# Kernel tuning notes

Hardware: AMD Instinct MI355X
Metric: run time of the kernel (lower is better)

The kernel has to match this reference:

```python
import jax, jax.numpy as jnp
import numpy as np

EPS = 1e-5  # BatchNorm2d default eps


def setup_inputs() -> dict:
    key = jax.random.key(0)
    k1, k2, k3, k4 = jax.random.split(key, 4)
    B, C, S, E = 2, 512, 256, 512  # C == E is required by the module's math
    x = jax.random.normal(k1, (B, C, S, E), dtype=jnp.float32)
    Q = jax.random.normal(k2, (E, E), dtype=jnp.float32)
    K = jax.random.normal(k3, (E, E), dtype=jnp.float32)
    V = jax.random.normal(k4, (E, E), dtype=jnp.float32)
    return {"x": x, "Q": Q, "K": K, "V": V}


def reference(x, Q, K, V):
    # BatchNorm2d(affine=False), training-mode batch stats over (B, H, W)
    mean = jnp.mean(x, axis=(0, 2, 3), keepdims=True)
    var = jnp.var(x, axis=(0, 2, 3), keepdims=True)  # biased, matches torch normalization
    xn = (x - mean) * jax.lax.rsqrt(var + EPS)

    divisor = jnp.sqrt(jnp.asarray(x.shape[-1], dtype=x.dtype))
    q = jnp.einsum('bcse,ef->bcsf', xn, Q)
    k = jnp.einsum('bcse,ef->bcsf', xn, K)
    v = jnp.einsum('bcse,ef->bcsf', xn, V)

    # scores: [B, C, S, S]
    prod = jnp.einsum('bcsf,bctf->bcst', q, k) / divisor
    # nn.Softmax2d softmaxes over the CHANNEL dim (axis 1)
    sm = jax.nn.softmax(prod, axis=1)
    attention = jnp.einsum('bcst,bctf->bcsf', sm, v)
    # dropout is identity in eval/reference mode; residual since E_in == E_out
    return attention + xn
```

## Files before the change

kernel.cpp:

```cpp
#include <hip/hip_runtime.h>
#include <hip/hip_bf16.h>
#include <cstdio>

#define Bn 2
#define Cn 512
#define Sn 256
#define En 512

typedef __attribute__((ext_vector_type(8))) short bf16x8;
typedef __attribute__((ext_vector_type(4))) float f32x4;

static constexpr size_t PROD_B = (1ull << 20);
static constexpr size_t V_B    = PROD_B + (256ull << 20);
static constexpr size_t ATH_B  = V_B + (256ull << 20);
static constexpr size_t ATL_B  = ATH_B + (512ull << 10);
static constexpr size_t VT_B   = ATL_B + (512ull << 10);
static constexpr size_t XNH_B  = VT_B + (512ull << 10);
static constexpr size_t XNL_B  = XNH_B + (256ull << 20);
static constexpr size_t WS_BIG = XNL_B + (256ull << 20);
static constexpr size_t SMT_B  = XNL_B;

__device__ __forceinline__ unsigned short f2bf(float f) {
  union { __hip_bfloat16 h; unsigned short u; } cv;
  cv.h = __float2bfloat16(f);
  return cv.u;
}
__device__ __forceinline__ float bf2f(unsigned short u) {
  union { unsigned int i; float f; } cv;
  cv.i = ((unsigned int)u) << 16;
  return cv.f;
}
__device__ __forceinline__ void split2(float v, unsigned short& h, unsigned short& l) {
  h = f2bf(v);
  l = f2bf(v - bf2f(h));
}
__device__ __forceinline__ int swzc(int row, int col) {
  return row * 64 + ((col & 3) | ((col & 60) ^ ((row & 7) << 3)));
}
__device__ __forceinline__ bf16x8 ldfrag(const unsigned short* arr, int row, int ks, int lane) {
  const int byte = (ks * 64 + ((lane >> 4) << 4)) ^ ((row & 7) << 4);
  return *(const bf16x8*)((const char*)(arr + (size_t)row * 64) + byte);
}
__device__ __forceinline__ f32x4 MFMA(bf16x8 a, bf16x8 b, f32x4 c) {
  return __builtin_amdgcn_mfma_f32_16x16x32_bf16(a, b, c, 0, 0, 0);
}
__device__ __forceinline__ void glds16(const void* g, void* l) {
  __builtin_amdgcn_global_load_lds(
      (const __attribute__((address_space(1))) unsigned int*)g,
      (__attribute__((address_space(3))) unsigned int*)l, 16, 0, 0);
}
__device__ __forceinline__ void stage_tile(const unsigned short* g, unsigned short* l,
                                           int nbytes, int wid, int lane, int nwaves) {
  const char* gb = (const char*)g;
  char* lb = (char*)l;
  for (int j = wid; j < (nbytes >> 10); j += nwaves)
    glds16(gb + j * 1024 + lane * 16, lb + j * 1024);
}

__global__ void k1_stats(const float* __restrict__ x, float* __restrict__ ws) {
  const int c = blockIdx.x, tid = threadIdx.x;
  const float4* p0 = (const float4*)(x + (size_t)c * (Sn * En));
  const float4* p1 = (const float4*)(x + (size_t)(Cn + c) * (Sn * En));
  float s1 = 0.f, s2 = 0.f;
  for (int i = tid; i < (Sn * En / 4); i += 256) {
    float4 a = p0[i], b = p1[i];
    s1 += (a.x + a.y) + (a.z + a.w) + (b.x + b.y) + (b.z + b.w);
    s2 += (a.x * a.x + a.y * a.y) + (a.z * a.z + a.w * a.w) +
          (b.x * b.x + b.y * b.y) + (b.z * b.z + b.w * b.w);
  }
  __shared__ float r1[256], r2[256];
  r1[tid] = s1; r2[tid] = s2;
  __syncthreads();
  for (int off = 128; off > 0; off >>= 1) {
    if (tid < off) { r1[tid] += r1[tid + off]; r2[tid] += r2[tid + off]; }
    __syncthreads();
  }
  if (tid == 0) {
    const float n = (float)(2 * Sn * En);
    float mean = r1[0] / n;
    float var = r2[0] / n - mean * mean;
    ws[c] = mean;
    ws[512 + c] = 1.0f / sqrtf(var + 1e-5f);
  }
}

__global__ void kA(const float* __restrict__ Q, const float* __restrict__ K,
                   const float* __restrict__ V, unsigned short* __restrict__ ATh,
                   unsigned short* __restrict__ ATl, unsigned short* __restrict__ VT) {
  const int f = blockIdx.x, tid = threadIdx.x;
  __shared__ float Kf[512];
  for (int i = tid; i < 512; i += 256) Kf[i] = K[(size_t)f * 512 + i];
  __syncthreads();
  const int fr64 = f & 63;
  const size_t atbase = ((size_t)(f >> 6) * 8) * 4096 + (size_t)fr64 * 64;
  const size_t vtbase = ((size_t)(f >> 7) * 8) * 8192 + (size_t)(f & 127) * 64;
#pragma unroll
  for (int half = 0; half < 2; ++half) {
    const int e = tid + half * 256;
    const float* Qe = Q + (size_t)e * 512;
    float acc = 0.f;
    for (int t = 0; t < 512; t += 4) {
      float4 q = *(const float4*)(Qe + t);
      acc += q.x * Kf[t] + q.y * Kf[t + 1] + q.z * Kf[t + 2] + q.w * Kf[t + 3];
    }
    unsigned short h, l;
    split2(acc, h, l);
    const int et = e >> 6, ec = e & 63;
    const int swa = (ec & 3) | ((ec & 60) ^ ((fr64 & 7) << 3));
    ATh[atbase + (size_t)et * 4096 + swa] = h;
    ATl[atbase + (size_t)et * 4096 + swa] = l;
    const int swv = (ec & 3) | ((ec & 60) ^ ((f & 7) << 3));
    VT[vtbase + (size_t)et * 8192 + swv] = f2bf(V[(size_t)e * 512 + f]);
  }
}

__global__ void kxn(const float* __restrict__ x, const float* __restrict__ ws,
                    unsigned short* __restrict__ XNh, unsigned short* __restrict__ XNl) {
  const int bid = blockIdx.x;
  const int bc = bid >> 1, half = bid & 1;
  const int c = bc & 511;
  const float mean = ws[c], rstd = ws[512 + c];
  const float* xb = x + (size_t)bc * 131072 + (size_t)half * 128 * 512;
  const int tid = threadIdx.x;
#pragma unroll 4
  for (int i = 0; i < 64; ++i) {
    const int g = tid + i * 256;
    const int r = g >> 7, c4 = g & 127;
    const float4 xv = *(const float4*)(xb + (size_t)r * 512 + c4 * 4);
    ushort4 hv, lv;
    split2((xv.x - mean) * rstd, hv.x, lv.x);
    split2((xv.y - mean) * rstd, hv.y, lv.y);
    split2((xv.z - mean) * rstd, hv.z, lv.z);
    split2((xv.w - mean) * rstd, hv.w, lv.w);
    const int et = c4 >> 4, colt4 = c4 & 15;
    const int row = half * 128 + r;
    const size_t idx = ((size_t)(bc * 8 + et) * 256 + row) * 64 +
                       ((colt4 * 4) ^ ((row & 7) << 3));
    *(ushort4*)&XNh[idx] = hv;
    *(ushort4*)&XNl[idx] = lv;
  }
}

__launch_bounds__(256)
__global__ void kv_proj(const unsigned short* __restrict__ VT,
                        const unsigned short* __restrict__ XNh_g,
                        unsigned short* __restrict__ vT_out) {
  __shared__ unsigned short BUF[2][16384];
  const int bid = blockIdx.x;
  const int L = (bid & 7) * 1024 + (bid >> 3);
  const int bc = L >> 3;
  const int fq = (L >> 1) & 3;
  const int th = L & 1;
  const int f0 = fq * 128, t0 = th * 128;
  const int tid = threadIdx.x, w = tid >> 6, lane = tid & 63;

  f32x4 acc[2][8];
#pragma unroll
  for (int i = 0; i < 2; ++i)
#pragma unroll
    for (int j = 0; j < 8; ++j) acc[i][j] = (f32x4){0.f, 0.f, 0.f, 0.f};

  stage_tile(VT + ((size_t)fq * 8 + 0) * 8192, &BUF[0][0], 16384, w, lane, 4);
  stage_tile(XNh_g + ((size_t)(bc * 8 + 0) * 256 + t0) * 64, &BUF[0][8192], 16384, w, lane, 4);
  __syncthreads();
#pragma unroll 1
  for (int et = 0; et < 8; ++et) {
    if (et < 7) {
      const int b = (et + 1) & 1;
      stage_tile(VT + ((size_t)fq * 8 + et + 1) * 8192, &BUF[b][0], 16384, w, lane, 4);
      stage_tile(XNh_g + ((size_t)(bc * 8 + et + 1) * 256 + t0) * 64, &BUF[b][8192],
                 16384, w, lane, 4);
    }
    const unsigned short* cb = &BUF[et & 1][0];
#pragma unroll
    for (int ks = 0; ks < 2; ++ks) {
      bf16x8 a0 = ldfrag(cb, w * 32 + (lane & 15), ks, lane);
      bf16x8 a1 = ldfrag(cb, w * 32 + 16 + (lane & 15), ks, lane);
#pragma unroll
      for (int ct = 0; ct < 8; ++ct) {
        bf16x8 b = ldfrag(cb + 8192, ct * 16 + (lane & 15), ks, lane);
        acc[0][ct] = MFMA(a0, b, acc[0][ct]);
        acc[1][ct] = MFMA(a1, b, acc[1][ct]);
      }
    }
    __syncthreads();
  }
#pragma unroll
  for (int rt = 0; rt < 2; ++rt)
#pragma unroll
    for (int ct = 0; ct < 8; ++ct)
#pragma unroll
      for (int r = 0; r < 4; ++r) {
        const int f = f0 + w * 32 + rt * 16 + (lane >> 4) * 4 + r;
        const int t = t0 + ct * 16 + (lane & 15);
        const size_t idx = (((size_t)bc * 4 + (f >> 7)) * 4 + (t >> 6)) * 8192 +
                           (size_t)(f & 127) * 64 +
                           ((t & 3) | ((t & 60) ^ ((f & 7) << 3)));
        vT_out[idx] = f2bf(acc[rt][ct][r]);
      }
}

__launch_bounds__(512, 2)
__global__ void kscores(const unsigned short* __restrict__ ATh_g,
                        const unsigned short* __restrict__ ATl_g,
                        const unsigned short* __restrict__ XNh_g,
                        const unsigned short* __restrict__ XNl_g,
                        float* __restrict__ prod) {
  __shared__ unsigned short STG[2][16384];
  __shared__ unsigned short YS[8][2048];
  const int bid = blockIdx.x;
  const int L = (bid & 7) * 256 + (bid >> 3);
  const int bc = L >> 1, half = L & 1;
  float* prodc = prod + (size_t)bc * 65536 + (size_t)half * 128 * 256;
  const int tid = threadIdx.x, w = tid >> 6, lane = tid & 63;
  const int lr = lane & 15, lk = lane >> 4;

  const int arow = half * 128 + w * 16 + lr;
  const unsigned short* xnh_row = XNh_g + ((size_t)bc * 8 * 256 + arow) * 64;
  const unsigned short* xnl_row = XNl_g + ((size_t)bc * 8 * 256 + arow) * 64;
  const int ac0 = (lk * 8) ^ ((arow & 7) << 3);
  const int ac1 = (32 + lk * 8) ^ ((arow & 7) << 3);

  f32x4 accz[16];
#pragma unroll
  for (int i = 0; i < 16; ++i) accz[i] = (f32x4){0.f, 0.f, 0.f, 0.f};
  f32x4 accy[4];
  unsigned short* const ys = &YS[w][0];

  auto stAT2 = [&](int ftx, int et2, int p) {
    stage_tile(ATh_g + ((size_t)ftx * 8 + et2) * 4096, STG[p], 16384, w, lane, 8);
    stage_tile(ATl_g + ((size_t)ftx * 8 + et2) * 4096, STG[p] + 8192, 16384, w, lane, 8);
  };
  auto stXT2 = [&](int ftx, int th, int p) {
    stage_tile(XNh_g + ((size_t)(bc * 8 + ftx) * 256 + th * 128) * 64, STG[p],
               16384, w, lane, 8);
    stage_tile(XNl_g + ((size_t)(bc * 8 + ftx) * 256 + th * 128) * 64, STG[p] + 8192,
               16384, w, lane, 8);
  };
  auto ph1pair = [&](int et2, int p) {
    __builtin_amdgcn_s_setprio(1);
#pragma unroll
    for (int e2 = 0; e2 < 2; ++e2) {
      const unsigned short* Bh = STG[p] + e2 * 4096;
      const unsigned short* Bl = STG[p] + 8192 + e2 * 4096;
      const size_t abase = (size_t)(et2 + e2) * 16384;
#pragma unroll
      for (int ks = 0; ks < 2; ++ks) {
        const int ac = ks ? ac1 : ac0;
        const bf16x8 ah = *(const bf16x8*)(xnh_row + abase + ac);
        const bf16x8 al = *(const bf16x8*)(xnl_row + abase + ac);
#pragma unroll
        for (int fc = 0; fc < 4; ++fc) {
          bf16x8 bh = ldfrag(Bh, fc * 16 + lr, ks, lane);
          bf16x8 bl = ldfrag(Bl, fc * 16 + lr, ks, lane);
          accy[fc] = MFMA(ah, bh, accy[fc]);
          accy[fc] = MFMA(ah, bl, accy[fc]);
          accy[fc] = MFMA(al, bh, accy[fc]);
        }
      }
    }
    __builtin_amdgcn_s_setprio(0);
  };
  auto ph2half = [&](int z0, int p) {
    __builtin_amdgcn_s_setprio(1);
#pragma unroll
    for (int ks = 0; ks < 2; ++ks) {
      bf16x8 yh = ldfrag(ys, lr, ks, lane);
      bf16x8 yl = ldfrag(ys + 1024, lr, ks, lane);
#pragma unroll
      for (int j = 0; j < 8; ++j) {
        bf16x8 bh = ldfrag(STG[p], j * 16 + lr, ks, lane);
        bf16x8 bl = ldfrag(STG[p] + 8192, j * 16 + lr, ks, lane);
        accz[z0 + j] = MFMA(yh, bh, accz[z0 + j]);
        accz[z0 + j] = MFMA(yh, bl, accz[z0 + j]);
        accz[z0 + j] = MFMA(yl, bh, accz[z0 + j]);
      }
    }
    __builtin_amdgcn_s_setprio(0);
  };
  auto ywrite = [&]() {
#pragma unroll
    for (int fc = 0; fc < 4; ++fc)
#pragma unroll
      for (int r = 0; r < 4; ++r) {
        const int row = lk * 4 + r;
        const int col = fc * 16 + lr;
        unsigned short h, l;
        split2(accy[fc][r], h, l);
        const int idx = swzc(row, col);
        ys[idx] = h;
        ys[1024 + idx] = l;
      }
  };

  stAT2(0, 0, 0);
  __syncthreads();

#pragma unroll 1
  for (int ft = 0; ft < 8; ++ft) {
#pragma unroll
    for (int i = 0; i < 4; ++i) accy[i] = (f32x4){0.f, 0.f, 0.f, 0.f};
    stAT2(ft, 2, 1);                 ph1pair(0, 0); __syncthreads();
    stAT2(ft, 4, 0);                 ph1pair(2, 1); __syncthreads();
    stAT2(ft, 6, 1);                 ph1pair(4, 0); __syncthreads();
    stXT2(ft, 0, 0);                 ph1pair(6, 1); __syncthreads();
    ywrite();
    stXT2(ft, 1, 1);                 ph2half(0, 0); __syncthreads();
    if (ft < 7) stAT2(ft + 1, 0, 0); ph2half(8, 1); __syncthreads();
  }

  const float scale = 0.044194173824159216f;
#pragma unroll
  for (int th = 0; th < 2; ++th)
#pragma unroll
    for (int ct = 0; ct < 8; ++ct)
#pragma unroll
      for (int r = 0; r < 4; ++r) {
        const int row = w * 16 + lk * 4 + r;
        prodc[(size_t)row * 256 + th * 128 + ct * 16 + lr] =
            accz[th * 8 + ct][r] * scale;
      }
}

__launch_bounds__(512)
__global__ void k3_softmax(const float* __restrict__ prodf, unsigned short* __restrict__ smT) {
  const int bid = blockIdx.x;
  const int b = bid >> 8, s = bid & 255;
  const int tid = threadIdx.x;
  const int t = tid & 255, ch = tid >> 8;
  const float* __restrict__ p =
      prodf + (size_t)b * (512ull * 65536) + (size_t)s * 256 + t + (size_t)ch * 256 * 65536;
  float m = -3.4e38f, sum = 0.f;
#pragma unroll 4
  for (int cc = 0; cc < 256; ++cc) {
    const float v = p[(size_t)cc * 65536];
    if (v > m) { sum *= __expf(m - v); m = v; }
    sum += __expf(v - m);
  }
  __shared__ float Ms[2][256], Ss[2][256];
  Ms[ch][t] = m; Ss[ch][t] = sum;
  __syncthreads();
  const float mo = Ms[ch ^ 1][t], so = Ss[ch ^ 1][t];
  const float mm = fmaxf(m, mo);
  const float inv = 1.0f / (sum * __expf(m - mm) + so * __expf(mo - mm));
  const int sh = s >> 7, r = s & 127, kt = t >> 6, col = t & 63;
  const int cidx = r * 64 + ((col & 3) | ((col & 60) ^ ((r & 7) << 3)));
  const size_t tbase = ((size_t)b * 512 + ch * 256) * 2 + sh;
#pragma unroll 4
  for (int cc = 0; cc < 256; ++cc) {
    const float ev = __expf(p[(size_t)cc * 65536] - mm) * inv;
    smT[((tbase + (size_t)cc * 2) * 4 + kt) * 8192 + cidx] = f2bf(ev);
  }
}

__launch_bounds__(256)
__global__ void k4_pv(const unsigned short* __restrict__ XNh_g,
                      const unsigned short* __restrict__ vT,
                      const unsigned short* __restrict__ smT,
                      float* __restrict__ out) {
  __shared__ unsigned short BUF[2][16384];
  const int bid = blockIdx.x;
  const int L = (bid & 7) * 1024 + (bid >> 3);
  const int bc = L >> 3;
  const int sh = (L >> 2) & 1;
  const int fh = L & 3;
  const int s0 = sh * 128, f0 = fh * 128;
  const int tid = threadIdx.x, w = tid >> 6, lane = tid & 63;

  f32x4 acc[2][8];
#pragma unroll
  for (int i = 0; i < 2; ++i)
#pragma unroll
    for (int j = 0; j < 8; ++j) acc[i][j] = (f32x4){0.f, 0.f, 0.f, 0.f};

  stage_tile(smT + (((size_t)bc * 2 + sh) * 4 + 0) * 8192, &BUF[0][0], 16384, w, lane, 4);
  stage_tile(vT + (((size_t)bc * 4 + fh) * 4 + 0) * 8192, &BUF[0][8192], 16384, w, lane, 4);
  __syncthreads();
#pragma unroll 1
  for (int kt = 0; kt < 4; ++kt) {
    if (kt < 3) {
      const int b = (kt + 1) & 1;
      stage_tile(smT + (((size_t)bc * 2 + sh) * 4 + kt + 1) * 8192, &BUF[b][0],
                 16384, w, lane, 4);
      stage_tile(vT + (((size_t)bc * 4 + fh) * 4 + kt + 1) * 8192, &BUF[b][8192],
                 16384, w, lane, 4);
    }
    const unsigned short* cb = &BUF[kt & 1][0];
#pragma unroll
    for (int ks = 0; ks < 2; ++ks) {
      bf16x8 a0 = ldfrag(cb, w * 32 + (lane & 15), ks, lane);
      bf16x8 a1 = ldfrag(cb, w * 32 + 16 + (lane & 15), ks, lane);
#pragma unroll
      for (int ct = 0; ct < 8; ++ct) {
        bf16x8 b = ldfrag(cb + 8192, ct * 16 + (lane & 15), ks, lane);
        acc[0][ct] = MFMA(a0, b, acc[0][ct]);
        acc[1][ct] = MFMA(a1, b, acc[1][ct]);
      }
    }
    __syncthreads();
  }
  const int lr = lane & 15, lk = lane >> 4;
#pragma unroll
  for (int rt = 0; rt < 2; ++rt)
#pragma unroll
    for (int ct = 0; ct < 8; ++ct)
#pragma unroll
      for (int r = 0; r < 4; ++r) {
        const int srow = s0 + w * 32 + rt * 16 + lk * 4 + r;
        const int fcol = f0 + ct * 16 + lr;
        const int et = fcol >> 6, col = fcol & 63;
        const unsigned short xh = XNh_g[((size_t)(bc * 8 + et) * 256 + srow) * 64 +
                                        ((col & 3) | ((col & 60) ^ ((srow & 7) << 3)))];
        const size_t oi = (size_t)bc * 131072 + (size_t)srow * 512 + fcol;
        out[oi] = acc[rt][ct][r] + bf2f(xh);
      }
}

extern "C" void kernel_launch(void* const* d_in, const int* in_sizes, int n_in,
                              void* d_out, int out_size, void* d_ws, size_t ws_size,
                              hipStream_t stream) {
  const float* x = (const float*)d_in[0];
  const float* Q = (const float*)d_in[1];
  const float* K = (const float*)d_in[2];
  const float* V = (const float*)d_in[3];
  float* out = (float*)d_out;
  float* ws = (float*)d_ws;
  float* prodf = (float*)((char*)d_ws + PROD_B);
  unsigned short* vT   = (unsigned short*)((char*)d_ws + V_B);
  unsigned short* ATh  = (unsigned short*)((char*)d_ws + ATH_B);
  unsigned short* ATl  = (unsigned short*)((char*)d_ws + ATL_B);
  unsigned short* VTm  = (unsigned short*)((char*)d_ws + VT_B);
  unsigned short* XNh  = (unsigned short*)((char*)d_ws + XNH_B);
  unsigned short* XNl  = (unsigned short*)((char*)d_ws + XNL_B);
  unsigned short* smT  = (unsigned short*)((char*)d_ws + SMT_B);
  if (ws_size < WS_BIG) {
    fprintf(stderr, "kernel_launch: ws_size %zu < needed %zu — expect corruption\n",
            ws_size, WS_BIG);
  }
  k1_stats<<<dim3(512), dim3(256), 0, stream>>>(x, ws);
  kA<<<dim3(512), dim3(256), 0, stream>>>(Q, K, V, ATh, ATl, VTm);
  kxn<<<dim3(2048), dim3(256), 0, stream>>>(x, ws, XNh, XNl);
  kv_proj<<<dim3(8192), dim3(256), 0, stream>>>(VTm, XNh, vT);
  kscores<<<dim3(2048), dim3(512), 0, stream>>>(ATh, ATl, XNh, XNl, prodf);
  k3_softmax<<<dim3(512), dim3(512), 0, stream>>>(prodf, smT);
  k4_pv<<<dim3(8192), dim3(256), 0, stream>>>(XNh, vT, smT, out);
}
```

Measured before the change: 1.880 ms.

## Triple-buffer kscores LDS staging with explicit vmcnt waits and A-fragment prefetch

The scores kernel moves from a double-buffered LDS staging ring to a triple-buffered one. `__syncthreads` is replaced by explicit `s_waitcnt vmcnt(4)` plus barrier, so the next tile's global-to-LDS loads stay in flight while the current tile is consumed. The xn A-fragments for each phase-1 pair are loaded into registers ahead of the MFMA loop instead of inside it. The extra 32KB of LDS and the dropped min-blocks launch bound likely cut occupancy to one block per CU, trading latency hiding across blocks for deeper in-block pipelining.

```diff
diff --git a/kernel.cpp b/kernel.cpp
--- a/kernel.cpp
+++ b/kernel.cpp
@@ -56,6 +56,14 @@
   for (int j = wid; j < (nbytes >> 10); j += nwaves)
     glds16(gb + j * 1024 + lane * 16, lb + j * 1024);
 }
+
+#define WAITB(N)                                                   \
+  do {                                                             \
+    asm volatile("s_waitcnt vmcnt(" #N ")" ::: "memory");          \
+    asm volatile("s_waitcnt lgkmcnt(0)" ::: "memory");             \
+    __builtin_amdgcn_s_barrier();                                  \
+    __builtin_amdgcn_sched_barrier(0);                             \
+  } while (0)
 
 __global__ void k1_stats(const float* __restrict__ x, float* __restrict__ ws) {
   const int c = blockIdx.x, tid = threadIdx.x;
@@ -200,13 +208,13 @@
       }
 }
 
-__launch_bounds__(512, 2)
+__launch_bounds__(512)
 __global__ void kscores(const unsigned short* __restrict__ ATh_g,
                         const unsigned short* __restrict__ ATl_g,
                         const unsigned short* __restrict__ XNh_g,
                         const unsigned short* __restrict__ XNl_g,
                         float* __restrict__ prod) {
-  __shared__ unsigned short STG[2][16384];
+  __shared__ unsigned short STG[3][16384];
   __shared__ unsigned short YS[8][2048];
   const int bid = blockIdx.x;
   const int L = (bid & 7) * 256 + (bid >> 3);
@@ -225,43 +233,50 @@
 #pragma unroll
   for (int i = 0; i < 16; ++i) accz[i] = (f32x4){0.f, 0.f, 0.f, 0.f};
   f32x4 accy[4];
+  bf16x8 A[2][2][2];
   unsigned short* const ys = &YS[w][0];
 
-  auto stAT2 = [&](int ftx, int et2, int p) {
-    stage_tile(ATh_g + ((size_t)ftx * 8 + et2) * 4096, STG[p], 16384, w, lane, 8);
-    stage_tile(ATl_g + ((size_t)ftx * 8 + et2) * 4096, STG[p] + 8192, 16384, w, lane, 8);
-  };
-  auto stXT2 = [&](int ftx, int th, int p) {
-    stage_tile(XNh_g + ((size_t)(bc * 8 + ftx) * 256 + th * 128) * 64, STG[p],
+  auto stAT2 = [&](int ftx, int et2, int slot) {
+    stage_tile(ATh_g + ((size_t)ftx * 8 + et2) * 4096, &STG[slot][0], 16384, w, lane, 8);
+    stage_tile(ATl_g + ((size_t)ftx * 8 + et2) * 4096, &STG[slot][8192], 16384, w, lane, 8);
+  };
+  auto stXT2 = [&](int ftx, int th, int slot) {
+    stage_tile(XNh_g + ((size_t)(bc * 8 + ftx) * 256 + th * 128) * 64, &STG[slot][0],
                16384, w, lane, 8);
-    stage_tile(XNl_g + ((size_t)(bc * 8 + ftx) * 256 + th * 128) * 64, STG[p] + 8192,
+    stage_tile(XNl_g + ((size_t)(bc * 8 + ftx) * 256 + th * 128) * 64, &STG[slot][8192],
                16384, w, lane, 8);
   };
-  auto ph1pair = [&](int et2, int p) {
+  auto aload = [&](int et2) {
+#pragma unroll
+    for (int e2 = 0; e2 < 2; ++e2) {
+      const size_t ab = (size_t)(et2 + e2) * 16384;
+      A[e2][0][0] = *(const bf16x8*)(xnh_row + ab + ac0);
+      A[e2][0][1] = *(const bf16x8*)(xnl_row + ab + ac0);
+      A[e2][1][0] = *(const bf16x8*)(xnh_row + ab + ac1);
+      A[e2][1][1] = *(const bf16x8*)(xnl_row + ab + ac1);
+    }
+  };
+  auto ph1pair = [&](int slot) {
     __builtin_amdgcn_s_setprio(1);
 #pragma unroll
     for (int e2 = 0; e2 < 2; ++e2) {
-      const unsigned short* Bh = STG[p] + e2 * 4096;
-      const unsigned short* Bl = STG[p] + 8192 + e2 * 4096;
-      const size_t abase = (size_t)(et2 + e2) * 16384;
+      const unsigned short* Bh = &STG[slot][e2 * 4096];
+      const unsigned short* Bl = &STG[slot][8192 + e2 * 4096];
 #pragma unroll
       for (int ks = 0; ks < 2; ++ks) {
-        const int ac = ks ? ac1 : ac0;
-        const bf16x8 ah = *(const bf16x8*)(xnh_row + abase + ac);
-        const bf16x8 al = *(const bf16x8*)(xnl_row + abase + ac);
 #pragma unroll
         for (int fc = 0; fc < 4; ++fc) {
           bf16x8 bh = ldfrag(Bh, fc * 16 + lr, ks, lane);
           bf16x8 bl = ldfrag(Bl, fc * 16 + lr, ks, lane);
-          accy[fc] = MFMA(ah, bh, accy[fc]);
-          accy[fc] = MFMA(ah, bl, accy[fc]);
-          accy[fc] = MFMA(al, bh, accy[fc]);
+          accy[fc] = MFMA(A[e2][ks][0], bh, accy[fc]);
+          accy[fc] = MFMA(A[e2][ks][0], bl, accy[fc]);
+          accy[fc] = MFMA(A[e2][ks][1], bh, accy[fc]);
         }
       }
     }
     __builtin_amdgcn_s_setprio(0);
   };
-  auto ph2half = [&](int z0, int p) {
+  auto ph2half = [&](int z0, int slot) {
     __builtin_amdgcn_s_setprio(1);
 #pragma unroll
     for (int ks = 0; ks < 2; ++ks) {
@@ -269,8 +284,8 @@
       bf16x8 yl = ldfrag(ys + 1024, lr, ks, lane);
 #pragma unroll
       for (int j = 0; j < 8; ++j) {
-        bf16x8 bh = ldfrag(STG[p], j * 16 + lr, ks, lane);
-        bf16x8 bl = ldfrag(STG[p] + 8192, j * 16 + lr, ks, lane);
+        bf16x8 bh = ldfrag(&STG[slot][0], j * 16 + lr, ks, lane);
+        bf16x8 bl = ldfrag(&STG[slot][8192], j * 16 + lr, ks, lane);
         accz[z0 + j] = MFMA(yh, bh, accz[z0 + j]);
         accz[z0 + j] = MFMA(yh, bl, accz[z0 + j]);
         accz[z0 + j] = MFMA(yl, bh, accz[z0 + j]);
@@ -294,19 +309,26 @@
   };
 
   stAT2(0, 0, 0);
-  __syncthreads();
+  stAT2(0, 2, 1);
 
 #pragma unroll 1
   for (int ft = 0; ft < 8; ++ft) {
 #pragma unroll
     for (int i = 0; i < 4; ++i) accy[i] = (f32x4){0.f, 0.f, 0.f, 0.f};
-    stAT2(ft, 2, 1);                 ph1pair(0, 0); __syncthreads();
-    stAT2(ft, 4, 0);                 ph1pair(2, 1); __syncthreads();
-    stAT2(ft, 6, 1);                 ph1pair(4, 0); __syncthreads();
-    stXT2(ft, 0, 0);                 ph1pair(6, 1); __syncthreads();
-    ywrite();
-    stXT2(ft, 1, 1);                 ph2half(0, 0); __syncthreads();
-    if (ft < 7) stAT2(ft + 1, 0, 0); ph2half(8, 1); __syncthreads();
+    WAITB(4); aload(0); __builtin_amdgcn_sched_barrier(0);
+    stAT2(ft, 4, 2); ph1pair(0);
+    WAITB(4); aload(2); __builtin_amdgcn_sched_barrier(0);
+    stAT2(ft, 6, 0); ph1pair(1);
+    WAITB(4); aload(4); __builtin_amdgcn_sched_barrier(0);
+    stXT2(ft, 0, 1); ph1pair(2);
+    WAITB(4); aload(6); __builtin_amdgcn_sched_barrier(0);
+    stXT2(ft, 1, 2); ph1pair(0); ywrite();
+    WAITB(4);
+    if (ft < 7) stAT2(ft + 1, 0, 0);
+    ph2half(0, 1);
+    if (ft < 7) { WAITB(4); stAT2(ft + 1, 2, 1); }
+    else        { WAITB(0); }
+    ph2half(8, 2);
   }
 
   const float scale = 0.044194173824159216f;
```

Measured after the change: 2.078 ms. 1.11x slower.

## Store normalized x in MFMA fragment-native layout for direct register loads

Applied to the files above, without the earlier changes.

The normalization kernel now transposes x through shared memory and writes the bf16 hi/lo split in a layout that matches the MFMA operand fragment order, so each lane's 8 values are contiguous. The V-projection, scores and output kernels index this new layout and read fragments with plain 16-byte loads instead of swizzled ldfrag gathers. This targets uncoalesced global A-operand loads in the scores kernel and the swizzle arithmetic in shared-memory reads. In exchange kxn gains an LDS transpose with extra barriers, and the residual read in the output kernel becomes more scattered.

```diff
diff --git a/kernel.cpp b/kernel.cpp
--- a/kernel.cpp
+++ b/kernel.cpp
@@ -116,28 +116,45 @@
 
 __global__ void kxn(const float* __restrict__ x, const float* __restrict__ ws,
                     unsigned short* __restrict__ XNh, unsigned short* __restrict__ XNl) {
+  __shared__ float xt[128 * 33];
   const int bid = blockIdx.x;
   const int bc = bid >> 1, half = bid & 1;
   const int c = bc & 511;
   const float mean = ws[c], rstd = ws[512 + c];
   const float* xb = x + (size_t)bc * 131072 + (size_t)half * 128 * 512;
   const int tid = threadIdx.x;
-#pragma unroll 4
-  for (int i = 0; i < 64; ++i) {
-    const int g = tid + i * 256;
-    const int r = g >> 7, c4 = g & 127;
-    const float4 xv = *(const float4*)(xb + (size_t)r * 512 + c4 * 4);
-    ushort4 hv, lv;
-    split2((xv.x - mean) * rstd, hv.x, lv.x);
-    split2((xv.y - mean) * rstd, hv.y, lv.y);
-    split2((xv.z - mean) * rstd, hv.z, lv.z);
-    split2((xv.w - mean) * rstd, hv.w, lv.w);
-    const int et = c4 >> 4, colt4 = c4 & 15;
-    const int row = half * 128 + r;
-    const size_t idx = ((size_t)(bc * 8 + et) * 256 + row) * 64 +
-                       ((colt4 * 4) ^ ((row & 7) << 3));
-    *(ushort4*)&XNh[idx] = hv;
-    *(ushort4*)&XNl[idx] = lv;
+  const int lane6 = tid & 63;
+  const int row15 = lane6 & 15, e8 = lane6 >> 4;
+
+#pragma unroll 1
+  for (int e32 = 0; e32 < 16; ++e32) {
+    __syncthreads();
+#pragma unroll
+    for (int i = 0; i < 4; ++i) {
+      const int g = tid + i * 256;
+      const int r = g >> 3, c4 = g & 7;
+      const float4 v = *(const float4*)(xb + (size_t)r * 512 + e32 * 32 + c4 * 4);
+      float* d = &xt[r * 33 + c4 * 4];
+      d[0] = v.x; d[1] = v.y; d[2] = v.z; d[3] = v.w;
+    }
+    __syncthreads();
+#pragma unroll
+    for (int it = 0; it < 2; ++it) {
+      const int rg = (tid >> 6) + it * 4;
+      const int row = rg * 16 + row15;
+      const float* s = &xt[row * 33 + e8 * 8];
+      short hv[8], lv[8];
+#pragma unroll
+      for (int k = 0; k < 8; ++k) {
+        unsigned short h, l;
+        split2((s[k] - mean) * rstd, h, l);
+        hv[k] = (short)h; lv[k] = (short)l;
+      }
+      const size_t base =
+          ((((size_t)bc * 16 + e32) * 16) + half * 8 + rg) * 512 + (size_t)lane6 * 8;
+      *(bf16x8*)&XNh[base] = *(const bf16x8*)hv;
+      *(bf16x8*)&XNl[base] = *(const bf16x8*)lv;
+    }
   }
 }
 
@@ -160,25 +177,32 @@
 #pragma unroll
     for (int j = 0; j < 8; ++j) acc[i][j] = (f32x4){0.f, 0.f, 0.f, 0.f};
 
+  auto stXN = [&](int et, int b) {
+    stage_tile(XNh_g + (((size_t)bc * 16 + et * 2 + 0) * 16 + th * 8) * 512,
+               &BUF[b][8192], 8192, w, lane, 4);
+    stage_tile(XNh_g + (((size_t)bc * 16 + et * 2 + 1) * 16 + th * 8) * 512,
+               &BUF[b][12288], 8192, w, lane, 4);
+  };
+
   stage_tile(VT + ((size_t)fq * 8 + 0) * 8192, &BUF[0][0], 16384, w, lane, 4);
-  stage_tile(XNh_g + ((size_t)(bc * 8 + 0) * 256 + t0) * 64, &BUF[0][8192], 16384, w, lane, 4);
+  stXN(0, 0);
   __syncthreads();
 #pragma unroll 1
   for (int et = 0; et < 8; ++et) {
     if (et < 7) {
       const int b = (et + 1) & 1;
       stage_tile(VT + ((size_t)fq * 8 + et + 1) * 8192, &BUF[b][0], 16384, w, lane, 4);
-      stage_tile(XNh_g + ((size_t)(bc * 8 + et + 1) * 256 + t0) * 64, &BUF[b][8192],
-                 16384, w, lane, 4);
+      stXN(et + 1, b);
     }
     const unsigned short* cb = &BUF[et & 1][0];
+    const char* xnimg = (const char*)(cb + 8192);
 #pragma unroll
     for (int ks = 0; ks < 2; ++ks) {
       bf16x8 a0 = ldfrag(cb, w * 32 + (lane & 15), ks, lane);
       bf16x8 a1 = ldfrag(cb, w * 32 + 16 + (lane & 15), ks, lane);
 #pragma unroll
       for (int ct = 0; ct < 8; ++ct) {
-        bf16x8 b = ldfrag(cb + 8192, ct * 16 + (lane & 15), ks, lane);
+        bf16x8 b = *(const bf16x8*)(xnimg + ks * 8192 + ct * 1024 + lane * 16);
         acc[0][ct] = MFMA(a0, b, acc[0][ct]);
         acc[1][ct] = MFMA(a1, b, acc[1][ct]);
       }
@@ -215,11 +239,9 @@
   const int tid = threadIdx.x, w = tid >> 6, lane = tid & 63;
   const int lr = lane & 15, lk = lane >> 4;
 
-  const int arow = half * 128 + w * 16 + lr;
-  const unsigned short* xnh_row = XNh_g + ((size_t)bc * 8 * 256 + arow) * 64;
-  const unsigned short* xnl_row = XNl_g + ((size_t)bc * 8 * 256 + arow) * 64;
-  const int ac0 = (lk * 8) ^ ((arow & 7) << 3);
-  const int ac1 = (32 + lk * 8) ^ ((arow & 7) << 3);
+  const unsigned short* xnh_bc = XNh_g + ((size_t)bc * 256) * 512;
+  const unsigned short* xnl_bc = XNl_g + ((size_t)bc * 256) * 512;
+  const int asub = (half * 8 + w) * 512 + lane * 8;
 
   f32x4 accz[16];
 #pragma unroll
@@ -232,10 +254,14 @@
     stage_tile(ATl_g + ((size_t)ftx * 8 + et2) * 4096, STG[p] + 8192, 16384, w, lane, 8);
   };
   auto stXT2 = [&](int ftx, int th, int p) {
-    stage_tile(XNh_g + ((size_t)(bc * 8 + ftx) * 256 + th * 128) * 64, STG[p],
-               16384, w, lane, 8);
-    stage_tile(XNl_g + ((size_t)(bc * 8 + ftx) * 256 + th * 128) * 64, STG[p] + 8192,
-               16384, w, lane, 8);
+    stage_tile(XNh_g + (((size_t)bc * 16 + ftx * 2 + 0) * 16 + th * 8) * 512,
+               STG[p], 8192, w, lane, 8);
+    stage_tile(XNh_g + (((size_t)bc * 16 + ftx * 2 + 1) * 16 + th * 8) * 512,
+               STG[p] + 4096, 8192, w, lane, 8);
+    stage_tile(XNl_g + (((size_t)bc * 16 + ftx * 2 + 0) * 16 + th * 8) * 512,
+               STG[p] + 8192, 8192, w, lane, 8);
+    stage_tile(XNl_g + (((size_t)bc * 16 + ftx * 2 + 1) * 16 + th * 8) * 512,
+               STG[p] + 12288, 8192, w, lane, 8);
   };
   auto ph1pair = [&](int et2, int p) {
     __builtin_amdgcn_s_setprio(1);
@@ -243,12 +269,11 @@
     for (int e2 = 0; e2 < 2; ++e2) {
       const unsigned short* Bh = STG[p] + e2 * 4096;
       const unsigned short* Bl = STG[p] + 8192 + e2 * 4096;
-      const size_t abase = (size_t)(et2 + e2) * 16384;
 #pragma unroll
       for (int ks = 0; ks < 2; ++ks) {
-        const int ac = ks ? ac1 : ac0;
-        const bf16x8 ah = *(const bf16x8*)(xnh_row + abase + ac);
-        const bf16x8 al = *(const bf16x8*)(xnl_row + abase + ac);
+        const size_t ch = (size_t)((et2 + e2) * 2 + ks) * 8192;
+        const bf16x8 ah = *(const bf16x8*)(xnh_bc + ch + asub);
+        const bf16x8 al = *(const bf16x8*)(xnl_bc + ch + asub);
 #pragma unroll
         for (int fc = 0; fc < 4; ++fc) {
           bf16x8 bh = ldfrag(Bh, fc * 16 + lr, ks, lane);
@@ -262,6 +287,7 @@
     __builtin_amdgcn_s_setprio(0);
   };
   auto ph2half = [&](int z0, int p) {
+    const char* sb = (const char*)&STG[p][0];
     __builtin_amdgcn_s_setprio(1);
 #pragma unroll
     for (int ks = 0; ks < 2; ++ks) {
@@ -269,8 +295,8 @@
       bf16x8 yl = ldfrag(ys + 1024, lr, ks, lane);
 #pragma unroll
       for (int j = 0; j < 8; ++j) {
-        bf16x8 bh = ldfrag(STG[p], j * 16 + lr, ks, lane);
-        bf16x8 bl = ldfrag(STG[p] + 8192, j * 16 + lr, ks, lane);
+        bf16x8 bh = *(const bf16x8*)(sb + ks * 8192 + j * 1024 + lane * 16);
+        bf16x8 bl = *(const bf16x8*)(sb + 16384 + ks * 8192 + j * 1024 + lane * 16);
         accz[z0 + j] = MFMA(yh, bh, accz[z0 + j]);
         accz[z0 + j] = MFMA(yh, bl, accz[z0 + j]);
         accz[z0 + j] = MFMA(yl, bh, accz[z0 + j]);
@@ -408,9 +434,10 @@
       for (int r = 0; r < 4; ++r) {
         const int srow = s0 + w * 32 + rt * 16 + lk * 4 + r;
         const int fcol = f0 + ct * 16 + lr;
-        const int et = fcol >> 6, col = fcol & 63;
-        const unsigned short xh = XNh_g[((size_t)(bc * 8 + et) * 256 + srow) * 64 +
-                                        ((col & 3) | ((col & 60) ^ ((srow & 7) << 3)))];
+        const int e32 = fcol >> 5, e8 = (fcol >> 3) & 3, el = fcol & 7;
+        const unsigned short xh =
+            XNh_g[(((size_t)bc * 16 + e32) * 16 + (srow >> 4)) * 512 +
+                  ((srow & 15) + e8 * 16) * 8 + el];
         const size_t oi = (size_t)bc * 131072 + (size_t)srow * 512 + fcol;
         out[oi] = acc[rt][ct][r] + bf2f(xh);
       }
```

Measured after the change: 1.969 ms. 4.7% more time.

## Loop kv_proj over all f-quarters per block and recompute residual from x

Applied to the files above, without the earlier changes.

The kv_proj kernel now has each block iterate over all four 128-wide f-quarters instead of launching one block per quarter. The block count drops by four and the pipelined staging runs continuously across the quarters, so more work sits between launch overheads. The PV kernel's residual now recomputes the normalized x in fp32 from x and the batch stats instead of reading the swizzled bf16 XNh copy. This improves residual precision and replaces a scattered bf16 gather with a coalesced fp32 read, but it doubles the bytes read for the residual.

```diff
diff --git a/kernel.cpp b/kernel.cpp
--- a/kernel.cpp
+++ b/kernel.cpp
@@ -147,57 +147,61 @@
                         unsigned short* __restrict__ vT_out) {
   __shared__ unsigned short BUF[2][16384];
   const int bid = blockIdx.x;
-  const int L = (bid & 7) * 1024 + (bid >> 3);
-  const int bc = L >> 3;
-  const int fq = (L >> 1) & 3;
+  const int L = (bid & 7) * 256 + (bid >> 3);
+  const int bc = L >> 1;
   const int th = L & 1;
-  const int f0 = fq * 128, t0 = th * 128;
+  const int t0 = th * 128;
   const int tid = threadIdx.x, w = tid >> 6, lane = tid & 63;
 
-  f32x4 acc[2][8];
-#pragma unroll
-  for (int i = 0; i < 2; ++i)
-#pragma unroll
-    for (int j = 0; j < 8; ++j) acc[i][j] = (f32x4){0.f, 0.f, 0.f, 0.f};
-
-  stage_tile(VT + ((size_t)fq * 8 + 0) * 8192, &BUF[0][0], 16384, w, lane, 4);
-  stage_tile(XNh_g + ((size_t)(bc * 8 + 0) * 256 + t0) * 64, &BUF[0][8192], 16384, w, lane, 4);
+  auto stage_pair = [&](int fq, int et, int b) {
+    stage_tile(VT + ((size_t)fq * 8 + et) * 8192, &BUF[b][0], 16384, w, lane, 4);
+    stage_tile(XNh_g + ((size_t)(bc * 8 + et) * 256 + t0) * 64, &BUF[b][8192],
+               16384, w, lane, 4);
+  };
+
+  stage_pair(0, 0, 0);
   __syncthreads();
 #pragma unroll 1
-  for (int et = 0; et < 8; ++et) {
-    if (et < 7) {
-      const int b = (et + 1) & 1;
-      stage_tile(VT + ((size_t)fq * 8 + et + 1) * 8192, &BUF[b][0], 16384, w, lane, 4);
-      stage_tile(XNh_g + ((size_t)(bc * 8 + et + 1) * 256 + t0) * 64, &BUF[b][8192],
-                 16384, w, lane, 4);
-    }
-    const unsigned short* cb = &BUF[et & 1][0];
-#pragma unroll
-    for (int ks = 0; ks < 2; ++ks) {
-      bf16x8 a0 = ldfrag(cb, w * 32 + (lane & 15), ks, lane);
-      bf16x8 a1 = ldfrag(cb, w * 32 + 16 + (lane & 15), ks, lane);
-#pragma unroll
-      for (int ct = 0; ct < 8; ++ct) {
-        bf16x8 b = ldfrag(cb + 8192, ct * 16 + (lane & 15), ks, lane);
-        acc[0][ct] = MFMA(a0, b, acc[0][ct]);
-        acc[1][ct] = MFMA(a1, b, acc[1][ct]);
-      }
-    }
-    __syncthreads();
-  }
-#pragma unroll
-  for (int rt = 0; rt < 2; ++rt)
-#pragma unroll
-    for (int ct = 0; ct < 8; ++ct)
-#pragma unroll
-      for (int r = 0; r < 4; ++r) {
-        const int f = f0 + w * 32 + rt * 16 + (lane >> 4) * 4 + r;
-        const int t = t0 + ct * 16 + (lane & 15);
-        const size_t idx = (((size_t)bc * 4 + (f >> 7)) * 4 + (t >> 6)) * 8192 +
-                           (size_t)(f & 127) * 64 +
-                           ((t & 3) | ((t & 60) ^ ((f & 7) << 3)));
-        vT_out[idx] = f2bf(acc[rt][ct][r]);
-      }
+  for (int fq = 0; fq < 4; ++fq) {
+    const int f0 = fq * 128;
+    f32x4 acc[2][8];
+#pragma unroll
+    for (int i = 0; i < 2; ++i)
+#pragma unroll
+      for (int j = 0; j < 8; ++j) acc[i][j] = (f32x4){0.f, 0.f, 0.f, 0.f};
+
+#pragma unroll 1
+    for (int et = 0; et < 8; ++et) {
+      const int idx = fq * 8 + et;
+      if (idx < 31) stage_pair((idx + 1) >> 3, (idx + 1) & 7, (idx + 1) & 1);
+      const unsigned short* cb = &BUF[idx & 1][0];
+#pragma unroll
+      for (int ks = 0; ks < 2; ++ks) {
+        bf16x8 a0 = ldfrag(cb, w * 32 + (lane & 15), ks, lane);
+        bf16x8 a1 = ldfrag(cb, w * 32 + 16 + (lane & 15), ks, lane);
+#pragma unroll
+        for (int ct = 0; ct < 8; ++ct) {
+          bf16x8 b = ldfrag(cb + 8192, ct * 16 + (lane & 15), ks, lane);
+          acc[0][ct] = MFMA(a0, b, acc[0][ct]);
+          acc[1][ct] = MFMA(a1, b, acc[1][ct]);
+        }
+      }
+      __syncthreads();
+    }
+#pragma unroll
+    for (int rt = 0; rt < 2; ++rt)
+#pragma unroll
+      for (int ct = 0; ct < 8; ++ct)
+#pragma unroll
+        for (int r = 0; r < 4; ++r) {
+          const int f = f0 + w * 32 + rt * 16 + (lane >> 4) * 4 + r;
+          const int t = t0 + ct * 16 + (lane & 15);
+          const size_t idx = (((size_t)bc * 4 + (f >> 7)) * 4 + (t >> 6)) * 8192 +
+                             (size_t)(f & 127) * 64 +
+                             ((t & 3) | ((t & 60) ^ ((f & 7) << 3)));
+          vT_out[idx] = f2bf(acc[rt][ct][r]);
+        }
+  }
 }
 
 __launch_bounds__(512, 2)
@@ -354,7 +358,7 @@
 }
 
 __launch_bounds__(256)
-__global__ void k4_pv(const unsigned short* __restrict__ XNh_g,
+__global__ void k4_pv(const float* __restrict__ x, const float* __restrict__ ws,
                       const unsigned short* __restrict__ vT,
                       const unsigned short* __restrict__ smT,
                       float* __restrict__ out) {
@@ -364,6 +368,8 @@
   const int bc = L >> 3;
   const int sh = (L >> 2) & 1;
   const int fh = L & 3;
+  const int c = bc & 511;
+  const float mean = ws[c], rstd = ws[512 + c];
   const int s0 = sh * 128, f0 = fh * 128;
   const int tid = threadIdx.x, w = tid >> 6, lane = tid & 63;
 
@@ -408,11 +414,8 @@
       for (int r = 0; r < 4; ++r) {
         const int srow = s0 + w * 32 + rt * 16 + lk * 4 + r;
         const int fcol = f0 + ct * 16 + lr;
-        const int et = fcol >> 6, col = fcol & 63;
-        const unsigned short xh = XNh_g[((size_t)(bc * 8 + et) * 256 + srow) * 64 +
-                                        ((col & 3) | ((col & 60) ^ ((srow & 7) << 3)))];
         const size_t oi = (size_t)bc * 131072 + (size_t)srow * 512 + fcol;
-        out[oi] = acc[rt][ct][r] + bf2f(xh);
+        out[oi] = acc[rt][ct][r] + (x[oi] - mean) * rstd;
       }
 }
 
@@ -440,8 +443,8 @@
   k1_stats<<<dim3(512), dim3(256), 0, stream>>>(x, ws);
   kA<<<dim3(512), dim3(256), 0, stream>>>(Q, K, V, ATh, ATl, VTm);
   kxn<<<dim3(2048), dim3(256), 0, stream>>>(x, ws, XNh, XNl);
-  kv_proj<<<dim3(8192), dim3(256), 0, stream>>>(VTm, XNh, vT);
+  kv_proj<<<dim3(2048), dim3(256), 0, stream>>>(VTm, XNh, vT);
   kscores<<<dim3(2048), dim3(512), 0, stream>>>(ATh, ATl, XNh, XNl, prodf);
   k3_softmax<<<dim3(512), dim3(512), 0, stream>>>(prodf, smT);
-  k4_pv<<<dim3(8192), dim3(256), 0, stream>>>(XNh, vT, smT, out);
-}
+  k4_pv<<<dim3(8192), dim3(256), 0, stream>>>(x, ws, vT, smT, out);
+}
```

After: 1.916 ms. No clear change (+1.9%).
